# Kernel optimization log

Measured on AMD Instinct MI355X. Metric: run time of the kernel, lower is better.

## Reference

```python
import jax, jax.numpy as jnp
import numpy as np

NUM_HEADS = 16
KEY_DEPTH = 1024


def setup_inputs() -> dict:
    key = jax.random.key(0)
    ks = jax.random.split(key, 7)
    B, L, D = 2, 2048, 1024
    scale = 1.0 / np.sqrt(D)
    return {
        "query_antecedent": jax.random.normal(ks[0], (B, L, D), jnp.float32),
        "memory_antecedent": jax.random.normal(ks[1], (B, L, D), jnp.float32),
        "bias": jax.random.normal(ks[2], (1, 1, L, L), jnp.float32),
        "Wq": jax.random.normal(ks[3], (D, KEY_DEPTH), jnp.float32) * scale,
        "Wk": jax.random.normal(ks[4], (D, KEY_DEPTH), jnp.float32) * scale,
        "Wv": jax.random.normal(ks[5], (D, KEY_DEPTH), jnp.float32) * scale,
        "Wo": jax.random.normal(ks[6], (KEY_DEPTH, D), jnp.float32) * scale,
    }


def _split_heads(x, h):
    # [B, L, D] -> [B, H, L, D/H]
    b, l, d = x.shape
    return x.reshape(b, l, h, d // h).transpose(0, 2, 1, 3)


def reference(query_antecedent, memory_antecedent, bias, Wq, Wk, Wv, Wo):
    h = NUM_HEADS
    d_head = KEY_DEPTH // h
    q = _split_heads(query_antecedent @ Wq, h) * (d_head ** -0.5)
    k = _split_heads(memory_antecedent @ Wk, h)
    v = _split_heads(memory_antecedent @ Wv, h)
    # [B, H, Lq, Lk]
    logits = jnp.einsum("bhqd,bhkd->bhqk", q, k) + bias
    weights = jax.nn.softmax(logits, axis=-1)
    x = jnp.einsum("bhqk,bhkd->bhqd", weights, v)
    # combine heads: [B, H, L, d] -> [B, L, H*d]
    b, _, l, d = x.shape
    x = x.transpose(0, 2, 1, 3).reshape(b, l, h * d)
    return x @ Wo
```

## Files before the change

### kernel.cpp

```cpp
#include <hip/hip_runtime.h>
#include <hip/hip_bf16.h>


typedef __attribute__((ext_vector_type(8))) short short8;
typedef __attribute__((ext_vector_type(4))) float float4v;

#define BATCH 2
#define LSEQ 2048
#define DMODEL 1024
#define NHEADS 16
#define DHEAD 64
#define MROWS 4096
#define QKVLD 3072

__global__ __launch_bounds__(256)
void convert_kernel(const float* __restrict__ qa, const float* __restrict__ ma,
                    __hip_bfloat16* __restrict__ qo, __hip_bfloat16* __restrict__ mo)
{
    const size_t i = ((size_t)blockIdx.x * 256 + threadIdx.x) * 8;
    const float* src = blockIdx.y ? ma : qa;
    __hip_bfloat16* dst = blockIdx.y ? mo : qo;
    float4 v0 = *reinterpret_cast<const float4*>(src + i);
    float4 v1 = *reinterpret_cast<const float4*>(src + i + 4);
    union { __hip_bfloat16 h[8]; int4 v; } pk;
    pk.h[0] = (__hip_bfloat16)v0.x; pk.h[1] = (__hip_bfloat16)v0.y;
    pk.h[2] = (__hip_bfloat16)v0.z; pk.h[3] = (__hip_bfloat16)v0.w;
    pk.h[4] = (__hip_bfloat16)v1.x; pk.h[5] = (__hip_bfloat16)v1.y;
    pk.h[6] = (__hip_bfloat16)v1.z; pk.h[7] = (__hip_bfloat16)v1.w;
    *reinterpret_cast<int4*>(dst + i) = pk.v;
}

__global__ __launch_bounds__(256)
void transpose_w_kernel(const float* __restrict__ W0, const float* __restrict__ W1,
                        const float* __restrict__ W2, const float* __restrict__ W3,
                        __hip_bfloat16* __restrict__ T0, __hip_bfloat16* __restrict__ T1,
                        __hip_bfloat16* __restrict__ T2, __hip_bfloat16* __restrict__ T3)
{
    __shared__ __hip_bfloat16 T[64][68];

    const float* W; __hip_bfloat16* D;
    if      (blockIdx.z == 0) { W = W0; D = T0; }
    else if (blockIdx.z == 1) { W = W1; D = T1; }
    else if (blockIdx.z == 2) { W = W2; D = T2; }
    else                      { W = W3; D = T3; }

    const int t  = threadIdx.x;
    const int n0 = blockIdx.x * 64;
    const int k0 = blockIdx.y * 64;

#pragma unroll
    for (int p = 0; p < 4; ++p) {
        const int r = p * 16 + (t >> 4);
        const int c = (t & 15) * 4;
        float4 v = *reinterpret_cast<const float4*>(&W[(size_t)(k0 + r) * DMODEL + n0 + c]);
        union { __hip_bfloat16 h[4]; ushort4 v; } pk;
        pk.h[0] = (__hip_bfloat16)v.x; pk.h[1] = (__hip_bfloat16)v.y;
        pk.h[2] = (__hip_bfloat16)v.z; pk.h[3] = (__hip_bfloat16)v.w;
        *reinterpret_cast<ushort4*>(&T[r][c]) = pk.v;
    }
    __syncthreads();
#pragma unroll
    for (int p = 0; p < 2; ++p) {
        const int n  = p * 32 + (t & 31);
        const int kc = (t >> 5) * 8;
        union { __hip_bfloat16 h[8]; int4 v; } pk;
#pragma unroll
        for (int j = 0; j < 8; ++j) pk.h[j] = T[kc + j][n];
        *reinterpret_cast<int4*>(&D[(size_t)(n0 + n) * DMODEL + k0 + kc]) = pk.v;
    }
}

__global__ __launch_bounds__(256)
void gemm_bt_kernel(const __hip_bfloat16* __restrict__ A0,
                    const __hip_bfloat16* __restrict__ A1, int nsplit,
                    float alpha0, float alpha1,
                    const __hip_bfloat16* __restrict__ Bt,
                    float* __restrict__ Cf, __hip_bfloat16* __restrict__ Cb,
                    int K, int ldc)
{
    __shared__ __hip_bfloat16 As[128][40];
    __shared__ __hip_bfloat16 Bs[128][40];

    const int t    = threadIdx.x;
    const int w    = t >> 6;
    const int lane = t & 63;
    const int l15  = lane & 15;
    const int lq   = lane >> 4;
    const int m0   = blockIdx.y * 128;
    const int n0   = blockIdx.x * 128;
    const int wm   = (w >> 1) * 64;
    const int wn   = (w & 1) * 64;
    const int sr   = t >> 1;
    const int sc   = (t & 1) * 16;

    const __hip_bfloat16* A = (n0 < nsplit) ? A0 : A1;
    const float alpha = (n0 < nsplit) ? alpha0 : alpha1;

    float4v acc[4][4];
#pragma unroll
    for (int mi = 0; mi < 4; ++mi)
#pragma unroll
        for (int ni = 0; ni < 4; ++ni) acc[mi][ni] = (float4v){0.f, 0.f, 0.f, 0.f};

    const __hip_bfloat16* Arow = A  + (size_t)(m0 + sr) * K + sc;
    const __hip_bfloat16* Brow = Bt + (size_t)(n0 + sr) * K + sc;

    int4 a0 = *reinterpret_cast<const int4*>(Arow);
    int4 a1 = *reinterpret_cast<const int4*>(Arow + 8);
    int4 b0 = *reinterpret_cast<const int4*>(Brow);
    int4 b1 = *reinterpret_cast<const int4*>(Brow + 8);

    for (int k0 = 0; k0 < K; k0 += 32) {
        __syncthreads();
        *reinterpret_cast<int4*>(&As[sr][sc])     = a0;
        *reinterpret_cast<int4*>(&As[sr][sc + 8]) = a1;
        *reinterpret_cast<int4*>(&Bs[sr][sc])     = b0;
        *reinterpret_cast<int4*>(&Bs[sr][sc + 8]) = b1;
        const int kn = (k0 + 32 < K) ? k0 + 32 : k0;
        a0 = *reinterpret_cast<const int4*>(Arow + kn);
        a1 = *reinterpret_cast<const int4*>(Arow + kn + 8);
        b0 = *reinterpret_cast<const int4*>(Brow + kn);
        b1 = *reinterpret_cast<const int4*>(Brow + kn + 8);
        __syncthreads();

        short8 af[4], bf[4];
#pragma unroll
        for (int mi = 0; mi < 4; ++mi)
            af[mi] = *reinterpret_cast<const short8*>(&As[wm + mi * 16 + l15][lq * 8]);
#pragma unroll
        for (int ni = 0; ni < 4; ++ni)
            bf[ni] = *reinterpret_cast<const short8*>(&Bs[wn + ni * 16 + l15][lq * 8]);
#pragma unroll
        for (int mi = 0; mi < 4; ++mi)
#pragma unroll
            for (int ni = 0; ni < 4; ++ni)
                acc[mi][ni] = __builtin_amdgcn_mfma_f32_16x16x32_bf16(
                    af[mi], bf[ni], acc[mi][ni], 0, 0, 0);
    }

#pragma unroll
    for (int mi = 0; mi < 4; ++mi)
#pragma unroll
        for (int ni = 0; ni < 4; ++ni)
#pragma unroll
            for (int r = 0; r < 4; ++r) {
                const int row = m0 + wm + mi * 16 + lq * 4 + r;
                const int col = n0 + wn + ni * 16 + l15;
                const float v = acc[mi][ni][r] * alpha;
                if (Cf) Cf[(size_t)row * ldc + col] = v;
                else    Cb[(size_t)row * ldc + col] = (__hip_bfloat16)v;
            }
}

#define KSTR 68
#define PSTR 132

__global__ __launch_bounds__(256)
void attn_mfma_kernel(const __hip_bfloat16* __restrict__ QKV,
                      const float* __restrict__ bias,
                      __hip_bfloat16* __restrict__ X)
{
    __shared__ __hip_bfloat16 Ks[128][KSTR];
    __shared__ __hip_bfloat16 Vt[64][PSTR];
    __shared__ __hip_bfloat16 Ps[4][32][PSTR];

    const int t   = threadIdx.x;
    const int w   = t >> 6;
    const int l15 = t & 15;
    const int lq  = (t & 63) >> 4;

    const int bid = blockIdx.x;
    const int r8  = bid & 7;
    const int j   = bid >> 3;
    const int bh  = r8 + 8 * (j >> 4);
    const int q0  = (j & 15) * 128;
    const int b   = bh >> 4;
    const int h   = bh & 15;

    const __hip_bfloat16* Kb = QKV + (size_t)b * LSEQ * QKVLD + 1024 + h * DHEAD;
    const __hip_bfloat16* Vb = Kb + 1024;

    short8 aq[2][2];
#pragma unroll
    for (int g = 0; g < 2; ++g) {
        const __hip_bfloat16* qrow = QKV +
            (size_t)(b * LSEQ + q0 + w * 32 + g * 16 + l15) * QKVLD + h * DHEAD + lq * 8;
        aq[g][0] = *reinterpret_cast<const short8*>(qrow);
        aq[g][1] = *reinterpret_cast<const short8*>(qrow + 32);
    }

    float lpart[2][4];
    float4v o_acc[2][4];
#pragma unroll
    for (int g = 0; g < 2; ++g)
#pragma unroll
        for (int r = 0; r < 4; ++r) lpart[g][r] = 0.f;
#pragma unroll
    for (int g = 0; g < 2; ++g)
#pragma unroll
        for (int n = 0; n < 4; ++n) o_acc[g][n] = (float4v){0.f, 0.f, 0.f, 0.f};

    const int skey = t >> 2;
    const int sdh  = (t & 3) * 16;
    const int g2   = t & 3;

    int4 pk[2][2], pv[2][2];
#pragma unroll
    for (int rnd = 0; rnd < 2; ++rnd) {
        const int key = rnd * 64 + skey;
        const __hip_bfloat16* ks = Kb + (size_t)key * QKVLD + sdh;
        pk[rnd][0] = *reinterpret_cast<const int4*>(ks);
        pk[rnd][1] = *reinterpret_cast<const int4*>(ks + 8);
        const __hip_bfloat16* vs = Vb + (size_t)key * QKVLD + sdh;
        pv[rnd][0] = *reinterpret_cast<const int4*>(vs);
        pv[rnd][1] = *reinterpret_cast<const int4*>(vs + 8);
    }

    for (int kt = 0; kt < LSEQ / 128; ++kt) {
        const int k0 = kt * 128;
        __syncthreads();
#pragma unroll
        for (int rnd = 0; rnd < 2; ++rnd) {
            const int key = rnd * 64 + skey;
            *reinterpret_cast<int4*>(&Ks[key][sdh])     = pk[rnd][0];
            *reinterpret_cast<int4*>(&Ks[key][sdh + 8]) = pk[rnd][1];
            const __hip_bfloat16* vp0 = reinterpret_cast<const __hip_bfloat16*>(&pv[rnd][0]);
            const __hip_bfloat16* vp1 = reinterpret_cast<const __hip_bfloat16*>(&pv[rnd][1]);
            const int vcol = (((key >> 3) ^ g2) << 3) + (key & 7);
#pragma unroll
            for (int jj = 0; jj < 8; ++jj) Vt[sdh + jj][vcol]     = vp0[jj];
#pragma unroll
            for (int jj = 0; jj < 8; ++jj) Vt[sdh + 8 + jj][vcol] = vp1[jj];
        }
        {
            const int knext = (kt + 1 < LSEQ / 128) ? k0 + 128 : k0;
#pragma unroll
            for (int rnd = 0; rnd < 2; ++rnd) {
                const int key = knext + rnd * 64 + skey;
                const __hip_bfloat16* ks = Kb + (size_t)key * QKVLD + sdh;
                pk[rnd][0] = *reinterpret_cast<const int4*>(ks);
                pk[rnd][1] = *reinterpret_cast<const int4*>(ks + 8);
                const __hip_bfloat16* vs = Vb + (size_t)key * QKVLD + sdh;
                pv[rnd][0] = *reinterpret_cast<const int4*>(vs);
                pv[rnd][1] = *reinterpret_cast<const int4*>(vs + 8);
            }
        }
        __syncthreads();

        float4v s0[8], s1[8];
#pragma unroll
        for (int c = 0; c < 8; ++c) {
            s0[c] = (float4v){0.f, 0.f, 0.f, 0.f};
            s1[c] = (float4v){0.f, 0.f, 0.f, 0.f};
        }
#pragma unroll
        for (int c = 0; c < 8; ++c) {
            short8 bk0 = *reinterpret_cast<const short8*>(&Ks[c * 16 + l15][lq * 8]);
            short8 bk1 = *reinterpret_cast<const short8*>(&Ks[c * 16 + l15][32 + lq * 8]);
            s0[c] = __builtin_amdgcn_mfma_f32_16x16x32_bf16(aq[0][0], bk0, s0[c], 0, 0, 0);
            s0[c] = __builtin_amdgcn_mfma_f32_16x16x32_bf16(aq[0][1], bk1, s0[c], 0, 0, 0);
            s1[c] = __builtin_amdgcn_mfma_f32_16x16x32_bf16(aq[1][0], bk0, s1[c], 0, 0, 0);
            s1[c] = __builtin_amdgcn_mfma_f32_16x16x32_bf16(aq[1][1], bk1, s1[c], 0, 0, 0);
        }

#pragma unroll
        for (int g = 0; g < 2; ++g) {
            float4v* s = g ? s1 : s0;
            const float* bp = bias +
                (size_t)(q0 + w * 32 + g * 16 + lq * 4) * LSEQ + l15;
            float bv[8][4];
#pragma unroll
            for (int c = 0; c < 8; ++c)
#pragma unroll
                for (int r = 0; r < 4; ++r)
                    bv[c][r] = bp[(size_t)r * LSEQ + k0 + c * 16];
#pragma unroll
            for (int c = 0; c < 8; ++c)
#pragma unroll
                for (int r = 0; r < 4; ++r) {
                    const float p = __expf(s[c][r] + bv[c][r]);
                    lpart[g][r] += p;
                    Ps[w][g * 16 + lq * 4 + r][c * 16 + l15] = (__hip_bfloat16)p;
                }
        }

        asm volatile("s_waitcnt lgkmcnt(0)" ::: "memory");

#pragma unroll
        for (int kc = 0; kc < 4; ++kc) {
            short8 vt[4];
#pragma unroll
            for (int n = 0; n < 4; ++n) {
                const int blk = (kc * 4 + lq) ^ n;
                vt[n] = *reinterpret_cast<const short8*>(&Vt[n * 16 + l15][blk << 3]);
            }
#pragma unroll
            for (int g = 0; g < 2; ++g) {
                short8 ap = *reinterpret_cast<const short8*>(
                    &Ps[w][g * 16 + l15][kc * 32 + lq * 8]);
#pragma unroll
                for (int n = 0; n < 4; ++n)
                    o_acc[g][n] = __builtin_amdgcn_mfma_f32_16x16x32_bf16(
                        ap, vt[n], o_acc[g][n], 0, 0, 0);
            }
        }
    }

#pragma unroll
    for (int g = 0; g < 2; ++g)
#pragma unroll
        for (int r = 0; r < 4; ++r) {
#pragma unroll
            for (int off = 1; off < 16; off <<= 1)
                lpart[g][r] += __shfl_xor(lpart[g][r], off);
        }

#pragma unroll
    for (int g = 0; g < 2; ++g) {
        float inv[4];
#pragma unroll
        for (int r = 0; r < 4; ++r) inv[r] = 1.f / lpart[g][r];
#pragma unroll
        for (int n = 0; n < 4; ++n)
#pragma unroll
            for (int r = 0; r < 4; ++r)
                Ps[w][g * 16 + lq * 4 + r][n * 16 + l15] =
                    (__hip_bfloat16)(o_acc[g][n][r] * inv[r]);
    }
    asm volatile("s_waitcnt lgkmcnt(0)" ::: "memory");
    {
        const int lane = t & 63;
        const int rr   = lane >> 2;
        const int cc   = (lane & 3) * 16;
#pragma unroll
        for (int g = 0; g < 2; ++g) {
            const int row = q0 + w * 32 + g * 16 + rr;
            __hip_bfloat16* dst =
                X + (size_t)(b * LSEQ + row) * DMODEL + h * DHEAD + cc;
            *reinterpret_cast<int4*>(dst) =
                *reinterpret_cast<const int4*>(&Ps[w][g * 16 + rr][cc]);
            *reinterpret_cast<int4*>(dst + 8) =
                *reinterpret_cast<const int4*>(&Ps[w][g * 16 + rr][cc + 8]);
        }
    }
}

extern "C" void kernel_launch(void* const* d_in, const int* in_sizes, int n_in,
                              void* d_out, int out_size, void* d_ws, size_t ws_size,
                              hipStream_t stream)
{
    const float* qa   = (const float*)d_in[0];
    const float* ma   = (const float*)d_in[1];
    const float* bias = (const float*)d_in[2];
    const float* Wq   = (const float*)d_in[3];
    const float* Wk   = (const float*)d_in[4];
    const float* Wv   = (const float*)d_in[5];
    const float* Wo   = (const float*)d_in[6];
    float* out = (float*)d_out;

    char* wsb = (char*)d_ws;
    __hip_bfloat16* qa16 = (__hip_bfloat16*)(wsb);
    __hip_bfloat16* ma16 = (__hip_bfloat16*)(wsb + (8u << 20));
    __hip_bfloat16* Wt   = (__hip_bfloat16*)(wsb + (16u << 20));
    __hip_bfloat16* Wot  = (__hip_bfloat16*)(wsb + (22u << 20));
    __hip_bfloat16* QKVw = (__hip_bfloat16*)(wsb + (24u << 20));
    __hip_bfloat16* Xw   = qa16;

    convert_kernel<<<dim3(MROWS * DMODEL / (256 * 8), 2), 256, 0, stream>>>(
        qa, ma, qa16, ma16);

    transpose_w_kernel<<<dim3(16, 16, 4), 256, 0, stream>>>(
        Wq, Wk, Wv, Wo,
        Wt, Wt + (size_t)DMODEL * DMODEL, Wt + 2 * (size_t)DMODEL * DMODEL, Wot);

    gemm_bt_kernel<<<dim3(QKVLD / 128, MROWS / 128), 256, 0, stream>>>(
        qa16, ma16, DMODEL, 0.125f, 1.0f, Wt, nullptr, QKVw, DMODEL, QKVLD);

    attn_mfma_kernel<<<dim3(512), 256, 0, stream>>>(QKVw, bias, Xw);

    gemm_bt_kernel<<<dim3(DMODEL / 128, MROWS / 128), 256, 0, stream>>>(
        Xw, Xw, DMODEL + 1, 1.0f, 1.0f, Wot, out, nullptr, DMODEL, DMODEL);
}
```

Baseline: 278.5 us.

## Split QKV outputs, pre-transpose V, keep P in registers, use direct-to-LDS loads

The QKV GEMM now writes Q, K and a pre-transposed V into separate buffers, so the attention kernel no longer transposes V element by element in LDS. Attention computes S transposed (K times Q), so the exponentiated probabilities stay in registers as the B operand of a 16x16x16 MFMA against V. This drops the per-warp P staging through shared memory, and the bias is read with vectorized float4 loads. Both GEMMs use global_load_lds async copies into unpadded LDS tiles, but they wait on vmcnt(0) every iteration, which removes the register prefetch overlap and may cause LDS bank conflicts.

```diff
diff --git a/kernel.cpp b/kernel.cpp
--- a/kernel.cpp
+++ b/kernel.cpp
@@ -3,15 +3,16 @@
 
 
 typedef __attribute__((ext_vector_type(8))) short short8;
+typedef __attribute__((ext_vector_type(4))) short short4v;
 typedef __attribute__((ext_vector_type(4))) float float4v;
 
-#define BATCH 2
 #define LSEQ 2048
 #define DMODEL 1024
-#define NHEADS 16
-#define DHEAD 64
 #define MROWS 4096
-#define QKVLD 3072
+
+#define GLDS(g, l) __builtin_amdgcn_global_load_lds(                        \
+    (const __attribute__((address_space(1))) void*)(g),                     \
+    (__attribute__((address_space(3))) void*)(l), 16, 0, 0)
 
 __global__ __launch_bounds__(256)
 void convert_kernel(const float* __restrict__ qa, const float* __restrict__ ma,
@@ -71,15 +72,15 @@
 }
 
 __global__ __launch_bounds__(256)
-void gemm_bt_kernel(const __hip_bfloat16* __restrict__ A0,
-                    const __hip_bfloat16* __restrict__ A1, int nsplit,
-                    float alpha0, float alpha1,
-                    const __hip_bfloat16* __restrict__ Bt,
-                    float* __restrict__ Cf, __hip_bfloat16* __restrict__ Cb,
-                    int K, int ldc)
-{
-    __shared__ __hip_bfloat16 As[128][40];
-    __shared__ __hip_bfloat16 Bs[128][40];
+void gemm_qkv_kernel(const __hip_bfloat16* __restrict__ qa16,
+                     const __hip_bfloat16* __restrict__ ma16,
+                     const __hip_bfloat16* __restrict__ Wt,
+                     __hip_bfloat16* __restrict__ Qw,
+                     __hip_bfloat16* __restrict__ Kw,
+                     __hip_bfloat16* __restrict__ VTw)
+{
+    __shared__ __hip_bfloat16 As[128 * 32];
+    __shared__ __hip_bfloat16 Bs[128 * 32];
 
     const int t    = threadIdx.x;
     const int w    = t >> 6;
@@ -90,11 +91,10 @@
     const int n0   = blockIdx.x * 128;
     const int wm   = (w >> 1) * 64;
     const int wn   = (w & 1) * 64;
-    const int sr   = t >> 1;
-    const int sc   = (t & 1) * 16;
-
-    const __hip_bfloat16* A = (n0 < nsplit) ? A0 : A1;
-    const float alpha = (n0 < nsplit) ? alpha0 : alpha1;
+    const int srow = lane >> 2;
+    const int scol = (lane & 3) * 8;
+
+    const __hip_bfloat16* A = (n0 < 1024) ? qa16 : ma16;
 
     float4v acc[4][4];
 #pragma unroll
@@ -102,34 +102,24 @@
 #pragma unroll
         for (int ni = 0; ni < 4; ++ni) acc[mi][ni] = (float4v){0.f, 0.f, 0.f, 0.f};
 
-    const __hip_bfloat16* Arow = A  + (size_t)(m0 + sr) * K + sc;
-    const __hip_bfloat16* Brow = Bt + (size_t)(n0 + sr) * K + sc;
-
-    int4 a0 = *reinterpret_cast<const int4*>(Arow);
-    int4 a1 = *reinterpret_cast<const int4*>(Arow + 8);
-    int4 b0 = *reinterpret_cast<const int4*>(Brow);
-    int4 b1 = *reinterpret_cast<const int4*>(Brow + 8);
-
-    for (int k0 = 0; k0 < K; k0 += 32) {
-        __syncthreads();
-        *reinterpret_cast<int4*>(&As[sr][sc])     = a0;
-        *reinterpret_cast<int4*>(&As[sr][sc + 8]) = a1;
-        *reinterpret_cast<int4*>(&Bs[sr][sc])     = b0;
-        *reinterpret_cast<int4*>(&Bs[sr][sc + 8]) = b1;
-        const int kn = (k0 + 32 < K) ? k0 + 32 : k0;
-        a0 = *reinterpret_cast<const int4*>(Arow + kn);
-        a1 = *reinterpret_cast<const int4*>(Arow + kn + 8);
-        b0 = *reinterpret_cast<const int4*>(Brow + kn);
-        b1 = *reinterpret_cast<const int4*>(Brow + kn + 8);
+    for (int k0 = 0; k0 < 1024; k0 += 32) {
+        __syncthreads();
+#pragma unroll
+        for (int i = 0; i < 2; ++i) {
+            const int rr = (w * 2 + i) * 16 + srow;
+            GLDS(A  + (size_t)(m0 + rr) * 1024 + k0 + scol, &As[(w * 2 + i) * 512]);
+            GLDS(Wt + (size_t)(n0 + rr) * 1024 + k0 + scol, &Bs[(w * 2 + i) * 512]);
+        }
+        asm volatile("s_waitcnt vmcnt(0)" ::: "memory");
         __syncthreads();
 
         short8 af[4], bf[4];
 #pragma unroll
         for (int mi = 0; mi < 4; ++mi)
-            af[mi] = *reinterpret_cast<const short8*>(&As[wm + mi * 16 + l15][lq * 8]);
+            af[mi] = *reinterpret_cast<const short8*>(&As[(wm + mi * 16 + l15) * 32 + lq * 8]);
 #pragma unroll
         for (int ni = 0; ni < 4; ++ni)
-            bf[ni] = *reinterpret_cast<const short8*>(&Bs[wn + ni * 16 + l15][lq * 8]);
+            bf[ni] = *reinterpret_cast<const short8*>(&Bs[(wn + ni * 16 + l15) * 32 + lq * 8]);
 #pragma unroll
         for (int mi = 0; mi < 4; ++mi)
 #pragma unroll
@@ -138,6 +128,92 @@
                     af[mi], bf[ni], acc[mi][ni], 0, 0, 0);
     }
 
+    if (n0 < 2048) {
+        __hip_bfloat16* C = (n0 < 1024) ? Qw : Kw;
+        const int   nb = (n0 < 1024) ? n0 : n0 - 1024;
+        const float al = (n0 < 1024) ? 0.125f : 1.0f;
+#pragma unroll
+        for (int mi = 0; mi < 4; ++mi)
+#pragma unroll
+            for (int ni = 0; ni < 4; ++ni)
+#pragma unroll
+                for (int r = 0; r < 4; ++r) {
+                    const int row = m0 + wm + mi * 16 + lq * 4 + r;
+                    const int col = nb + wn + ni * 16 + l15;
+                    C[(size_t)row * 1024 + col] = (__hip_bfloat16)(acc[mi][ni][r] * al);
+                }
+    } else {
+#pragma unroll
+        for (int mi = 0; mi < 4; ++mi) {
+            const int rowbase = m0 + wm + mi * 16 + lq * 4;
+            const int b   = rowbase >> 11;
+            const int seq = rowbase & 2047;
+#pragma unroll
+            for (int ni = 0; ni < 4; ++ni) {
+                const int n = n0 - 2048 + wn + ni * 16 + l15;
+                const int h = n >> 6, d = n & 63;
+                union { __hip_bfloat16 hh[4]; uint2 v; } pk;
+#pragma unroll
+                for (int r = 0; r < 4; ++r) pk.hh[r] = (__hip_bfloat16)acc[mi][ni][r];
+                *reinterpret_cast<uint2*>(
+                    &VTw[((size_t)(b * 16 + h) * 64 + d) * 2048 + seq]) = pk.v;
+            }
+        }
+    }
+}
+
+__global__ __launch_bounds__(256)
+void gemm_out_kernel(const __hip_bfloat16* __restrict__ Xw,
+                     const __hip_bfloat16* __restrict__ Wot,
+                     float* __restrict__ out)
+{
+    __shared__ __hip_bfloat16 As[128 * 32];
+    __shared__ __hip_bfloat16 Bs[128 * 32];
+
+    const int t    = threadIdx.x;
+    const int w    = t >> 6;
+    const int lane = t & 63;
+    const int l15  = lane & 15;
+    const int lq   = lane >> 4;
+    const int m0   = blockIdx.y * 128;
+    const int n0   = blockIdx.x * 128;
+    const int wm   = (w >> 1) * 64;
+    const int wn   = (w & 1) * 64;
+    const int srow = lane >> 2;
+    const int scol = (lane & 3) * 8;
+
+    float4v acc[4][4];
+#pragma unroll
+    for (int mi = 0; mi < 4; ++mi)
+#pragma unroll
+        for (int ni = 0; ni < 4; ++ni) acc[mi][ni] = (float4v){0.f, 0.f, 0.f, 0.f};
+
+    for (int k0 = 0; k0 < 1024; k0 += 32) {
+        __syncthreads();
+#pragma unroll
+        for (int i = 0; i < 2; ++i) {
+            const int rr = (w * 2 + i) * 16 + srow;
+            GLDS(Xw  + (size_t)(m0 + rr) * 1024 + k0 + scol, &As[(w * 2 + i) * 512]);
+            GLDS(Wot + (size_t)(n0 + rr) * 1024 + k0 + scol, &Bs[(w * 2 + i) * 512]);
+        }
+        asm volatile("s_waitcnt vmcnt(0)" ::: "memory");
+        __syncthreads();
+
+        short8 af[4], bf[4];
+#pragma unroll
+        for (int mi = 0; mi < 4; ++mi)
+            af[mi] = *reinterpret_cast<const short8*>(&As[(wm + mi * 16 + l15) * 32 + lq * 8]);
+#pragma unroll
+        for (int ni = 0; ni < 4; ++ni)
+            bf[ni] = *reinterpret_cast<const short8*>(&Bs[(wn + ni * 16 + l15) * 32 + lq * 8]);
+#pragma unroll
+        for (int mi = 0; mi < 4; ++mi)
+#pragma unroll
+            for (int ni = 0; ni < 4; ++ni)
+                acc[mi][ni] = __builtin_amdgcn_mfma_f32_16x16x32_bf16(
+                    af[mi], bf[ni], acc[mi][ni], 0, 0, 0);
+    }
+
 #pragma unroll
     for (int mi = 0; mi < 4; ++mi)
 #pragma unroll
@@ -146,23 +222,19 @@
             for (int r = 0; r < 4; ++r) {
                 const int row = m0 + wm + mi * 16 + lq * 4 + r;
                 const int col = n0 + wn + ni * 16 + l15;
-                const float v = acc[mi][ni][r] * alpha;
-                if (Cf) Cf[(size_t)row * ldc + col] = v;
-                else    Cb[(size_t)row * ldc + col] = (__hip_bfloat16)v;
+                out[(size_t)row * 1024 + col] = acc[mi][ni][r];
             }
 }
 
-#define KSTR 68
-#define PSTR 132
-
 __global__ __launch_bounds__(256)
-void attn_mfma_kernel(const __hip_bfloat16* __restrict__ QKV,
-                      const float* __restrict__ bias,
-                      __hip_bfloat16* __restrict__ X)
-{
-    __shared__ __hip_bfloat16 Ks[128][KSTR];
-    __shared__ __hip_bfloat16 Vt[64][PSTR];
-    __shared__ __hip_bfloat16 Ps[4][32][PSTR];
+void attn_kernel(const __hip_bfloat16* __restrict__ Qw,
+                 const __hip_bfloat16* __restrict__ Kw,
+                 const __hip_bfloat16* __restrict__ VTw,
+                 const float* __restrict__ bias,
+                 __hip_bfloat16* __restrict__ X)
+{
+    __shared__ __hip_bfloat16 Ks[128][72];
+    __shared__ __hip_bfloat16 Vt[64][136];
 
     const int t   = threadIdx.x;
     const int w   = t >> 6;
@@ -177,170 +249,131 @@
     const int b   = bh >> 4;
     const int h   = bh & 15;
 
-    const __hip_bfloat16* Kb = QKV + (size_t)b * LSEQ * QKVLD + 1024 + h * DHEAD;
-    const __hip_bfloat16* Vb = Kb + 1024;
-
-    short8 aq[2][2];
+    const __hip_bfloat16* Kb  = Kw + (size_t)b * LSEQ * 1024 + h * 64;
+    const __hip_bfloat16* VTb = VTw + ((size_t)(b * 16 + h) * 64) * 2048;
+
+    short8 bq[2][2];
 #pragma unroll
     for (int g = 0; g < 2; ++g) {
-        const __hip_bfloat16* qrow = QKV +
-            (size_t)(b * LSEQ + q0 + w * 32 + g * 16 + l15) * QKVLD + h * DHEAD + lq * 8;
-        aq[g][0] = *reinterpret_cast<const short8*>(qrow);
-        aq[g][1] = *reinterpret_cast<const short8*>(qrow + 32);
-    }
-
-    float lpart[2][4];
-    float4v o_acc[2][4];
+        const __hip_bfloat16* qrow = Qw +
+            (size_t)(b * LSEQ + q0 + w * 32 + g * 16 + l15) * 1024 + h * 64 + lq * 8;
+        bq[g][0] = *reinterpret_cast<const short8*>(qrow);
+        bq[g][1] = *reinterpret_cast<const short8*>(qrow + 32);
+    }
+
+    float lpart[2] = {0.f, 0.f};
+    float4v o[2][4];
 #pragma unroll
     for (int g = 0; g < 2; ++g)
 #pragma unroll
-        for (int r = 0; r < 4; ++r) lpart[g][r] = 0.f;
-#pragma unroll
-    for (int g = 0; g < 2; ++g)
-#pragma unroll
-        for (int n = 0; n < 4; ++n) o_acc[g][n] = (float4v){0.f, 0.f, 0.f, 0.f};
+        for (int mi = 0; mi < 4; ++mi) o[g][mi] = (float4v){0.f, 0.f, 0.f, 0.f};
 
     const int skey = t >> 2;
     const int sdh  = (t & 3) * 16;
-    const int g2   = t & 3;
-
-    int4 pk[2][2], pv[2][2];
+    const int vd   = t >> 2;
+    const int vk   = (t & 3) * 32;
+
+    int4 pk_[2][2], pv_[4];
 #pragma unroll
     for (int rnd = 0; rnd < 2; ++rnd) {
-        const int key = rnd * 64 + skey;
-        const __hip_bfloat16* ks = Kb + (size_t)key * QKVLD + sdh;
-        pk[rnd][0] = *reinterpret_cast<const int4*>(ks);
-        pk[rnd][1] = *reinterpret_cast<const int4*>(ks + 8);
-        const __hip_bfloat16* vs = Vb + (size_t)key * QKVLD + sdh;
-        pv[rnd][0] = *reinterpret_cast<const int4*>(vs);
-        pv[rnd][1] = *reinterpret_cast<const int4*>(vs + 8);
-    }
+        const __hip_bfloat16* ks = Kb + (size_t)(rnd * 64 + skey) * 1024 + sdh;
+        pk_[rnd][0] = *reinterpret_cast<const int4*>(ks);
+        pk_[rnd][1] = *reinterpret_cast<const int4*>(ks + 8);
+    }
+#pragma unroll
+    for (int c = 0; c < 4; ++c)
+        pv_[c] = *reinterpret_cast<const int4*>(VTb + (size_t)vd * 2048 + vk + c * 8);
 
     for (int kt = 0; kt < LSEQ / 128; ++kt) {
         const int k0 = kt * 128;
         __syncthreads();
 #pragma unroll
         for (int rnd = 0; rnd < 2; ++rnd) {
-            const int key = rnd * 64 + skey;
-            *reinterpret_cast<int4*>(&Ks[key][sdh])     = pk[rnd][0];
-            *reinterpret_cast<int4*>(&Ks[key][sdh + 8]) = pk[rnd][1];
-            const __hip_bfloat16* vp0 = reinterpret_cast<const __hip_bfloat16*>(&pv[rnd][0]);
-            const __hip_bfloat16* vp1 = reinterpret_cast<const __hip_bfloat16*>(&pv[rnd][1]);
-            const int vcol = (((key >> 3) ^ g2) << 3) + (key & 7);
-#pragma unroll
-            for (int jj = 0; jj < 8; ++jj) Vt[sdh + jj][vcol]     = vp0[jj];
-#pragma unroll
-            for (int jj = 0; jj < 8; ++jj) Vt[sdh + 8 + jj][vcol] = vp1[jj];
-        }
+            *reinterpret_cast<int4*>(&Ks[rnd * 64 + skey][sdh])     = pk_[rnd][0];
+            *reinterpret_cast<int4*>(&Ks[rnd * 64 + skey][sdh + 8]) = pk_[rnd][1];
+        }
+#pragma unroll
+        for (int c = 0; c < 4; ++c)
+            *reinterpret_cast<int4*>(&Vt[vd][vk + c * 8]) = pv_[c];
         {
-            const int knext = (kt + 1 < LSEQ / 128) ? k0 + 128 : k0;
+            const int kn = (kt + 1 < LSEQ / 128) ? k0 + 128 : k0;
 #pragma unroll
             for (int rnd = 0; rnd < 2; ++rnd) {
-                const int key = knext + rnd * 64 + skey;
-                const __hip_bfloat16* ks = Kb + (size_t)key * QKVLD + sdh;
-                pk[rnd][0] = *reinterpret_cast<const int4*>(ks);
-                pk[rnd][1] = *reinterpret_cast<const int4*>(ks + 8);
-                const __hip_bfloat16* vs = Vb + (size_t)key * QKVLD + sdh;
-                pv[rnd][0] = *reinterpret_cast<const int4*>(vs);
-                pv[rnd][1] = *reinterpret_cast<const int4*>(vs + 8);
+                const __hip_bfloat16* ks = Kb + (size_t)(kn + rnd * 64 + skey) * 1024 + sdh;
+                pk_[rnd][0] = *reinterpret_cast<const int4*>(ks);
+                pk_[rnd][1] = *reinterpret_cast<const int4*>(ks + 8);
             }
-        }
-        __syncthreads();
-
-        float4v s0[8], s1[8];
+#pragma unroll
+            for (int c = 0; c < 4; ++c)
+                pv_[c] = *reinterpret_cast<const int4*>(VTb + (size_t)vd * 2048 + kn + vk + c * 8);
+        }
+        __syncthreads();
+
+        float4v s[2][8];
 #pragma unroll
         for (int c = 0; c < 8; ++c) {
-            s0[c] = (float4v){0.f, 0.f, 0.f, 0.f};
-            s1[c] = (float4v){0.f, 0.f, 0.f, 0.f};
+            s[0][c] = (float4v){0.f, 0.f, 0.f, 0.f};
+            s[1][c] = (float4v){0.f, 0.f, 0.f, 0.f};
         }
 #pragma unroll
         for (int c = 0; c < 8; ++c) {
-            short8 bk0 = *reinterpret_cast<const short8*>(&Ks[c * 16 + l15][lq * 8]);
-            short8 bk1 = *reinterpret_cast<const short8*>(&Ks[c * 16 + l15][32 + lq * 8]);
-            s0[c] = __builtin_amdgcn_mfma_f32_16x16x32_bf16(aq[0][0], bk0, s0[c], 0, 0, 0);
-            s0[c] = __builtin_amdgcn_mfma_f32_16x16x32_bf16(aq[0][1], bk1, s0[c], 0, 0, 0);
-            s1[c] = __builtin_amdgcn_mfma_f32_16x16x32_bf16(aq[1][0], bk0, s1[c], 0, 0, 0);
-            s1[c] = __builtin_amdgcn_mfma_f32_16x16x32_bf16(aq[1][1], bk1, s1[c], 0, 0, 0);
-        }
-
+            short8 ka0 = *reinterpret_cast<const short8*>(&Ks[c * 16 + l15][lq * 8]);
+            short8 ka1 = *reinterpret_cast<const short8*>(&Ks[c * 16 + l15][32 + lq * 8]);
+            s[0][c] = __builtin_amdgcn_mfma_f32_16x16x32_bf16(ka0, bq[0][0], s[0][c], 0, 0, 0);
+            s[0][c] = __builtin_amdgcn_mfma_f32_16x16x32_bf16(ka1, bq[0][1], s[0][c], 0, 0, 0);
+            s[1][c] = __builtin_amdgcn_mfma_f32_16x16x32_bf16(ka0, bq[1][0], s[1][c], 0, 0, 0);
+            s[1][c] = __builtin_amdgcn_mfma_f32_16x16x32_bf16(ka1, bq[1][1], s[1][c], 0, 0, 0);
+        }
+
+        short4v pb[2][8];
 #pragma unroll
         for (int g = 0; g < 2; ++g) {
-            float4v* s = g ? s1 : s0;
             const float* bp = bias +
-                (size_t)(q0 + w * 32 + g * 16 + lq * 4) * LSEQ + l15;
-            float bv[8][4];
-#pragma unroll
-            for (int c = 0; c < 8; ++c)
-#pragma unroll
-                for (int r = 0; r < 4; ++r)
-                    bv[c][r] = bp[(size_t)r * LSEQ + k0 + c * 16];
-#pragma unroll
-            for (int c = 0; c < 8; ++c)
+                (size_t)(q0 + w * 32 + g * 16 + l15) * LSEQ + k0 + lq * 4;
+#pragma unroll
+            for (int c = 0; c < 8; ++c) {
+                float4 bvv = *reinterpret_cast<const float4*>(bp + c * 16);
+                const float* bv = reinterpret_cast<const float*>(&bvv);
+                union { __hip_bfloat16 hh[4]; short4v v; } pkk;
+                float acc_l = 0.f;
 #pragma unroll
                 for (int r = 0; r < 4; ++r) {
-                    const float p = __expf(s[c][r] + bv[c][r]);
-                    lpart[g][r] += p;
-                    Ps[w][g * 16 + lq * 4 + r][c * 16 + l15] = (__hip_bfloat16)p;
+                    const float p = __expf(s[g][c][r] + bv[r]);
+                    acc_l += p;
+                    pkk.hh[r] = (__hip_bfloat16)p;
                 }
-        }
-
-        asm volatile("s_waitcnt lgkmcnt(0)" ::: "memory");
-
-#pragma unroll
-        for (int kc = 0; kc < 4; ++kc) {
-            short8 vt[4];
-#pragma unroll
-            for (int n = 0; n < 4; ++n) {
-                const int blk = (kc * 4 + lq) ^ n;
-                vt[n] = *reinterpret_cast<const short8*>(&Vt[n * 16 + l15][blk << 3]);
+                lpart[g] += acc_l;
+                pb[g][c] = pkk.v;
             }
-#pragma unroll
-            for (int g = 0; g < 2; ++g) {
-                short8 ap = *reinterpret_cast<const short8*>(
-                    &Ps[w][g * 16 + l15][kc * 32 + lq * 8]);
-#pragma unroll
-                for (int n = 0; n < 4; ++n)
-                    o_acc[g][n] = __builtin_amdgcn_mfma_f32_16x16x32_bf16(
-                        ap, vt[n], o_acc[g][n], 0, 0, 0);
+        }
+
+#pragma unroll
+        for (int mi = 0; mi < 4; ++mi) {
+#pragma unroll
+            for (int kk = 0; kk < 8; ++kk) {
+                short4v va = *reinterpret_cast<const short4v*>(
+                    &Vt[mi * 16 + l15][kk * 16 + lq * 4]);
+                o[0][mi] = __builtin_amdgcn_mfma_f32_16x16x16bf16_1k(
+                    va, pb[0][kk], o[0][mi], 0, 0, 0);
+                o[1][mi] = __builtin_amdgcn_mfma_f32_16x16x16bf16_1k(
+                    va, pb[1][kk], o[1][mi], 0, 0, 0);
             }
         }
     }
 
 #pragma unroll
-    for (int g = 0; g < 2; ++g)
-#pragma unroll
-        for (int r = 0; r < 4; ++r) {
-#pragma unroll
-            for (int off = 1; off < 16; off <<= 1)
-                lpart[g][r] += __shfl_xor(lpart[g][r], off);
-        }
-
-#pragma unroll
     for (int g = 0; g < 2; ++g) {
-        float inv[4];
-#pragma unroll
-        for (int r = 0; r < 4; ++r) inv[r] = 1.f / lpart[g][r];
-#pragma unroll
-        for (int n = 0; n < 4; ++n)
-#pragma unroll
-            for (int r = 0; r < 4; ++r)
-                Ps[w][g * 16 + lq * 4 + r][n * 16 + l15] =
-                    (__hip_bfloat16)(o_acc[g][n][r] * inv[r]);
-    }
-    asm volatile("s_waitcnt lgkmcnt(0)" ::: "memory");
-    {
-        const int lane = t & 63;
-        const int rr   = lane >> 2;
-        const int cc   = (lane & 3) * 16;
-#pragma unroll
-        for (int g = 0; g < 2; ++g) {
-            const int row = q0 + w * 32 + g * 16 + rr;
-            __hip_bfloat16* dst =
-                X + (size_t)(b * LSEQ + row) * DMODEL + h * DHEAD + cc;
-            *reinterpret_cast<int4*>(dst) =
-                *reinterpret_cast<const int4*>(&Ps[w][g * 16 + rr][cc]);
-            *reinterpret_cast<int4*>(dst + 8) =
-                *reinterpret_cast<const int4*>(&Ps[w][g * 16 + rr][cc + 8]);
+        float lp = lpart[g];
+        lp += __shfl_xor(lp, 16);
+        lp += __shfl_xor(lp, 32);
+        const float inv = 1.f / lp;
+        const size_t xrow = (size_t)(b * LSEQ + q0 + w * 32 + g * 16 + l15) * 1024;
+#pragma unroll
+        for (int mi = 0; mi < 4; ++mi) {
+            union { __hip_bfloat16 hh[4]; uint2 v; } pkk;
+#pragma unroll
+            for (int r = 0; r < 4; ++r) pkk.hh[r] = (__hip_bfloat16)(o[g][mi][r] * inv);
+            *reinterpret_cast<uint2*>(&X[xrow + h * 64 + mi * 16 + lq * 4]) = pkk.v;
         }
     }
 }
@@ -360,10 +393,12 @@
 
     char* wsb = (char*)d_ws;
     __hip_bfloat16* qa16 = (__hip_bfloat16*)(wsb);
-    __hip_bfloat16* ma16 = (__hip_bfloat16*)(wsb + (8u << 20));
+    __hip_bfloat16* ma16 = (__hip_bfloat16*)(wsb + (8u  << 20));
     __hip_bfloat16* Wt   = (__hip_bfloat16*)(wsb + (16u << 20));
     __hip_bfloat16* Wot  = (__hip_bfloat16*)(wsb + (22u << 20));
-    __hip_bfloat16* QKVw = (__hip_bfloat16*)(wsb + (24u << 20));
+    __hip_bfloat16* Qw   = (__hip_bfloat16*)(wsb + (24u << 20));
+    __hip_bfloat16* Kw   = (__hip_bfloat16*)(wsb + (32u << 20));
+    __hip_bfloat16* VTw  = (__hip_bfloat16*)(wsb + (40u << 20));
     __hip_bfloat16* Xw   = qa16;
 
     convert_kernel<<<dim3(MROWS * DMODEL / (256 * 8), 2), 256, 0, stream>>>(
@@ -373,11 +408,11 @@
         Wq, Wk, Wv, Wo,
         Wt, Wt + (size_t)DMODEL * DMODEL, Wt + 2 * (size_t)DMODEL * DMODEL, Wot);
 
-    gemm_bt_kernel<<<dim3(QKVLD / 128, MROWS / 128), 256, 0, stream>>>(
-        qa16, ma16, DMODEL, 0.125f, 1.0f, Wt, nullptr, QKVw, DMODEL, QKVLD);
-
-    attn_mfma_kernel<<<dim3(512), 256, 0, stream>>>(QKVw, bias, Xw);
-
-    gemm_bt_kernel<<<dim3(DMODEL / 128, MROWS / 128), 256, 0, stream>>>(
-        Xw, Xw, DMODEL + 1, 1.0f, 1.0f, Wot, out, nullptr, DMODEL, DMODEL);
-}
+    gemm_qkv_kernel<<<dim3(3072 / 128, MROWS / 128), 256, 0, stream>>>(
+        qa16, ma16, Wt, Qw, Kw, VTw);
+
+    attn_kernel<<<dim3(512), 256, 0, stream>>>(Qw, Kw, VTw, bias, Xw);
+
+    gemm_out_kernel<<<dim3(1024 / 128, MROWS / 128), 256, 0, stream>>>(
+        Xw, Wot, out);
+}
```

Result: slower. 403.6 us (+44.9%).
